# Kernel optimization log

Hardware: AMD Instinct MI355X
Metric: run time of the kernel (lower is better)

## Reference

```python
import jax, jax.numpy as jnp
import numpy as np

WINDOW_SIZE = 2
SOFTMAX_TEMP = 0.01


def get_indices(batch_size, window_size):
    # For each window, match keypoints of frame j against dense map of frame j+1.
    kp_inds, dense_inds = [], []
    for i in range(batch_size):
        for j in range(window_size - 1):
            idx = i * window_size + j
            kp_inds.append(idx)
            dense_inds.append(idx + 1)
    return np.array(kp_inds), np.array(dense_inds)


def l2_normalize(x, axis):
    n = jnp.sqrt(jnp.sum(x * x, axis=axis, keepdims=True))
    return x / jnp.maximum(n, 1e-12)


def grid_sample_bilinear(img, grid_u, grid_v):
    """torch.nn.functional.grid_sample, mode='bilinear', padding='zeros', align_corners=False.
    img: (B,C,H,W); grid_u, grid_v: (B,N) normalized coords in [-1,1]. Returns (B,C,N)."""
    B, C, H, W = img.shape
    x = ((grid_u + 1.0) * W - 1.0) * 0.5  # pixel x
    y = ((grid_v + 1.0) * H - 1.0) * 0.5  # pixel y
    x0 = jnp.floor(x)
    y0 = jnp.floor(y)
    wx1 = x - x0
    wy1 = y - y0
    flat = img.reshape(B, C, H * W)

    def gather(xi, yi):
        valid = (xi >= 0) & (xi <= W - 1) & (yi >= 0) & (yi <= H - 1)
        xi_c = jnp.clip(xi, 0, W - 1).astype(jnp.int32)
        yi_c = jnp.clip(yi, 0, H - 1).astype(jnp.int32)
        idx = yi_c * W + xi_c  # (B,N)
        vals = jnp.take_along_axis(flat, idx[:, None, :], axis=2)  # (B,C,N)
        return vals * valid[:, None, :].astype(img.dtype)

    out = (gather(x0, y0) * ((1 - wx1) * (1 - wy1))[:, None, :]
           + gather(x0 + 1, y0) * (wx1 * (1 - wy1))[:, None, :]
           + gather(x0, y0 + 1) * ((1 - wx1) * wy1)[:, None, :]
           + gather(x0 + 1, y0 + 1) * (wx1 * wy1)[:, None, :])
    return out


def setup_inputs() -> dict:
    key = jax.random.key(0)
    k1, k2, k3, k4 = jax.random.split(key, 4)
    BW, C, N, H, W = 8, 128, 512, 256, 256
    return {
        "keypoint_scores": jax.random.uniform(k1, (BW, 1, N), dtype=jnp.float32),
        "keypoint_desc": jax.random.normal(k2, (BW, C, N), dtype=jnp.float32),
        "scores_dense": jax.random.uniform(k3, (BW, 1, H, W), dtype=jnp.float32),
        "desc_dense": jax.random.normal(k4, (BW, C, H, W), dtype=jnp.float32),
    }


def reference(keypoint_scores, keypoint_desc, scores_dense, desc_dense):
    BW, C, N = keypoint_desc.shape
    batch_size = BW // WINDOW_SIZE
    _, _, H, W = desc_dense.shape
    kp_inds, dense_inds = get_indices(batch_size, WINDOW_SIZE)

    src_desc = l2_normalize(keypoint_desc[kp_inds], axis=1)  # (B,C,N)
    B = src_desc.shape[0]
    tgt_desc_dense = desc_dense[dense_inds]  # (B,C,H,W)
    tgt_unrolled = l2_normalize(tgt_desc_dense.reshape(B, C, H * W), axis=1)

    # cosine similarity scores (B,N,H*W) -> temperature softmax over dense map
    match_vals = jnp.einsum('bcn,bcm->bnm', src_desc, tgt_unrolled)
    soft_match_vals = jax.nn.softmax(match_vals / SOFTMAX_TEMP, axis=2)

    # soft-argmax: expected (u,v) pixel coordinates
    v_coord, u_coord = jnp.meshgrid(jnp.arange(H), jnp.arange(W), indexing='ij')
    coords = jnp.stack([u_coord.reshape(-1), v_coord.reshape(-1)], axis=1).astype(jnp.float32)  # (HW,2)
    pseudo_coords = jnp.einsum('bnm,mk->bnk', soft_match_vals, coords)  # (B,N,2)

    u_norm = 2.0 * pseudo_coords[:, :, 0] / (W - 1) - 1.0
    v_norm = 2.0 * pseudo_coords[:, :, 1] / (H - 1) - 1.0

    tgt_scores_dense = scores_dense[dense_inds]
    pseudo_scores = grid_sample_bilinear(tgt_scores_dense, u_norm, v_norm)  # (B,1,N)
    pseudo_desc = grid_sample_bilinear(tgt_desc_dense, u_norm, v_norm)      # (B,C,N)

    desc_match_score = jnp.sum(src_desc * pseudo_desc, axis=1, keepdims=True) / float(C)
    src_scores = keypoint_scores[kp_inds]
    match_weights = 0.5 * (desc_match_score + 1.0) * src_scores * pseudo_scores
    return (pseudo_coords, match_weights, soft_match_vals)
```

## Files before the change

kernel.cpp:

```cpp
#include <hip/hip_runtime.h>


typedef short  v8s __attribute__((ext_vector_type(8)));
typedef unsigned short v8u __attribute__((ext_vector_type(8)));
typedef float  v4f __attribute__((ext_vector_type(4)));

#define EXP2_SCALE 144.269504088896f
#define WAITV(N) asm volatile("s_waitcnt vmcnt(" #N ")" ::: "memory")
#define SBAR()   __builtin_amdgcn_s_barrier()
#define SCHED()  __builtin_amdgcn_sched_barrier(0)

static const size_t O_AHI  = 0;
static const size_t O_ALO  = O_AHI  + 262144ull*2;
static const size_t O_SRCN = O_ALO  + 262144ull*2;
static const size_t O_BHI  = O_SRCN + 262144ull*4;
static const size_t O_BLO  = O_BHI  + 33554432ull*2;
static const size_t O_PART = O_BLO  + 33554432ull*2;
static const size_t O_ROWS = O_PART + 2048ull*512*16;

static __device__ inline unsigned short f2bf(float x) {
    unsigned u = __float_as_uint(x);
    u = u + 0x7FFFu + ((u >> 16) & 1u);
    return (unsigned short)(u >> 16);
}
static __device__ inline float bf2f(unsigned short h) {
    return __uint_as_float(((unsigned)h) << 16);
}

__device__ __forceinline__ void gl_lds16(const void* g, void* l) {
    auto gp = (const __attribute__((address_space(1))) unsigned int*)(uintptr_t)g;
    auto lp = (__attribute__((address_space(3))) unsigned int*)(uintptr_t)l;
    __builtin_amdgcn_global_load_lds(gp, lp, 16, 0, 0);
}

__global__ void __launch_bounds__(256) k_prep_src(const float* __restrict__ kd,
                                                  float* __restrict__ srcN,
                                                  unsigned short* __restrict__ Ahi,
                                                  unsigned short* __restrict__ Alo) {
    int gw = blockIdx.x * 4 + (threadIdx.x >> 6);
    int l  = threadIdx.x & 63;
    int b  = gw >> 9, n = gw & 511;
    const float* base = kd + (size_t)(2 * b) * 128 * 512;
    float x0 = base[l * 512 + n];
    float x1 = base[(l + 64) * 512 + n];
    float ss = x0 * x0 + x1 * x1;
#pragma unroll
    for (int m = 1; m < 64; m <<= 1) ss += __shfl_xor(ss, m, 64);
    float inv = 1.0f / fmaxf(sqrtf(ss), 1e-12f);
    float xn0 = x0 * inv, xn1 = x1 * inv;
    int ob = gw * 128;
    srcN[ob + l] = xn0;  srcN[ob + l + 64] = xn1;
    unsigned short h0 = f2bf(xn0), h1 = f2bf(xn1);
    Ahi[ob + l] = h0;        Ahi[ob + l + 64] = h1;
    Alo[ob + l] = f2bf(xn0 - bf2f(h0));
    Alo[ob + l + 64] = f2bf(xn1 - bf2f(h1));
}

__global__ void __launch_bounds__(256) k_prep_tgt(const float* __restrict__ dd,
                                                  unsigned short* __restrict__ Bhi,
                                                  unsigned short* __restrict__ Blo) {
    int t = blockIdx.x * 128 + (threadIdx.x >> 1);
    int h = threadIdx.x & 1;
    int b = t >> 16;
    int p = t & 65535;
    const float* src = dd + (size_t)(2 * b + 1) * 128 * 65536 + (size_t)(h * 64) * 65536 + p;
    float v[64];
    float ss = 0.f;
#pragma unroll
    for (int c = 0; c < 64; ++c) { float x = src[(size_t)c * 65536]; v[c] = x; ss += x * x; }
    ss += __shfl_xor(ss, 1, 64);
    float inv = 1.0f / fmaxf(sqrtf(ss), 1e-12f);
    size_t ob = (size_t)t * 128 + h * 64;
#pragma unroll
    for (int c8 = 0; c8 < 8; ++c8) {
        v8u h8, l8;
#pragma unroll
        for (int j = 0; j < 8; ++j) {
            float xn = v[c8 * 8 + j] * inv;
            unsigned short hh = f2bf(xn);
            h8[j] = hh;
            l8[j] = f2bf(xn - bf2f(hh));
        }
        *(v8u*)(Bhi + ob + c8 * 8) = h8;
        *(v8u*)(Blo + ob + c8 * 8) = l8;
    }
}

template <int MODE>
__global__ void __launch_bounds__(512, 2) k_gemm(const unsigned short* __restrict__ Ahi,
                                                 const unsigned short* __restrict__ Alo,
                                                 const unsigned short* __restrict__ Bhi,
                                                 const unsigned short* __restrict__ Blo,
                                                 const float4* __restrict__ rows,
                                                 float* __restrict__ part,
                                                 float* __restrict__ out,
                                                 const float* __restrict__ ksc,
                                                 const float* __restrict__ sd,
                                                 const float* __restrict__ dd,
                                                 const float* __restrict__ srcN) {
    __shared__ v4f bstage4[6144];
    char* bstage = (char*)bstage4;

    const int tid = threadIdx.x;
    const int l = tid & 63, w = tid >> 6;
    const int wm = w >> 2, wn = w & 3;
    const int l15 = l & 15, l16 = l >> 4;
    const int mtg = blockIdx.x, ny = blockIdx.y, b = blockIdx.z;
    const int mt0 = mtg * 16;
    float* osm = out + 6144;

    v8s ahi[2][4], alo[2][4];
    {
        const size_t ar = ((size_t)(b * 512 + ny * 128 + wn * 32 + l15)) * 128 + l16 * 8;
#pragma unroll
        for (int nf = 0; nf < 2; ++nf)
#pragma unroll
            for (int ksl = 0; ksl < 4; ++ksl) {
                ahi[nf][ksl] = *(const v8s*)(Ahi + ar + nf * 2048 + ksl * 32);
                alo[nf][ksl] = *(const v8s*)(Alo + ar + nf * 2048 + ksl * 32);
            }
    }
    float invs[2];
    if (MODE == 1) {
#pragma unroll
        for (int nf = 0; nf < 2; ++nf)
            invs[nf] = rows[b * 512 + ny * 128 + wn * 32 + nf * 16 + l15].x;
    }
    WAITV(0);

    const size_t pxbase = ((size_t)b * 65536 + (size_t)mt0 * 128) * 128;

#define STAGEU(SRC, prow, bufidx)                                                   \
    {                                                                               \
        const unsigned short* src_ = (SRC) + (prow);                                \
        char* dst_ = bstage + (bufidx) * 32768;                                     \
        _Pragma("unroll")                                                           \
        for (int i = 0; i < 4; ++i) {                                               \
            int sl = tid + i * 512;                                                 \
            int rl = sl >> 4, gg = sl & 15;                                         \
            gl_lds16(src_ + rl * 128 + ((gg ^ (rl & 15)) << 3), dst_ + (sl << 4));  \
        }                                                                           \
    }
#define PXF(bufbase, mf_, ksl_)                                                     \
    (*(const v8s*)((bufbase) + (wm * 64 + (mf_) * 16 + l15) * 256 +                 \
                   ((((ksl_) * 4 + l16) ^ ((wm * 64 + (mf_) * 16 + l15) & 15)) << 4)))

    v4f acc[4][2];

    if (MODE == 0) {
        STAGEU(Bhi, pxbase, 0);
        STAGEU(Bhi, pxbase + 16384, 1);
#pragma unroll 1
        for (int mt = 0; mt < 16; ++mt) {
            if (mt < 14) STAGEU(Bhi, pxbase + (size_t)(mt + 2) * 16384, (mt + 2) % 3);
            if (mt == 0) WAITV(8);
            else if (mt == 1) WAITV(10);
            else if (mt == 14) WAITV(8);
            else if (mt == 15) WAITV(4);
            else WAITV(12);
            SBAR(); SCHED();
            const char* bb = bstage + (mt % 3) * 32768;
#pragma unroll
            for (int mf = 0; mf < 4; ++mf)
#pragma unroll
                for (int nf = 0; nf < 2; ++nf) { v4f z = {0.f,0.f,0.f,0.f}; acc[mf][nf] = z; }
#pragma unroll
            for (int ksl = 0; ksl < 4; ++ksl) {
                v8s pxf[4];
#pragma unroll
                for (int mf = 0; mf < 4; ++mf) pxf[mf] = PXF(bb, mf, ksl);
#pragma unroll
                for (int mf = 0; mf < 4; ++mf)
#pragma unroll
                    for (int nf = 0; nf < 2; ++nf) {
                        acc[mf][nf] = __builtin_amdgcn_mfma_f32_16x16x32_bf16(pxf[mf], ahi[nf][ksl], acc[mf][nf], 0, 0, 0);
                        acc[mf][nf] = __builtin_amdgcn_mfma_f32_16x16x32_bf16(pxf[mf], alo[nf][ksl], acc[mf][nf], 0, 0, 0);
                    }
            }
            SCHED();
            float sS[2] = {0.f, 0.f}, sM[2] = {0.f, 0.f};
#pragma unroll
            for (int mf = 0; mf < 4; ++mf) {
                int mloc = wm * 64 + mf * 16 + l16 * 4;
#pragma unroll
                for (int nf = 0; nf < 2; ++nf)
#pragma unroll
                    for (int r = 0; r < 4; ++r) {
                        float e = __builtin_amdgcn_exp2f(fmaf(acc[mf][nf][r], EXP2_SCALE, -EXP2_SCALE));
                        sS[nf] += e;
                        sM[nf] = fmaf(e, (float)(mloc + r), sM[nf]);
                    }
            }
#pragma unroll
            for (int nf = 0; nf < 2; ++nf) {
                sS[nf] += __shfl_xor(sS[nf], 16, 64); sS[nf] += __shfl_xor(sS[nf], 32, 64);
                sM[nf] += __shfl_xor(sM[nf], 16, 64); sM[nf] += __shfl_xor(sM[nf], 32, 64);
            }
            if (l < 16) {
#pragma unroll
                for (int nf = 0; nf < 2; ++nf) {
                    int row = b * 512 + ny * 128 + wn * 32 + nf * 16 + l15;
                    *(float2*)(part + (((size_t)row * 512 + (mt0 + mt)) * 2 + wm) * 2)
                        = make_float2(sS[nf], sM[nf]);
                }
            }
            SBAR();
        }
    } else {
        STAGEU(Bhi, pxbase, 0);
        STAGEU(Blo, pxbase, 1);
#pragma unroll 1
        for (int ph = 0; ph < 32; ++ph) {
            if (ph < 30) {
                size_t prow2 = pxbase + (size_t)((ph + 2) >> 1) * 16384;
                if ((ph & 1) == 0) STAGEU(Bhi, prow2, (ph + 2) % 3)
                else               STAGEU(Blo, prow2, (ph + 2) % 3)
            }
            if (ph <= 1) WAITV(8);
            else if (ph == 30) WAITV(12);
            else if (ph == 31) WAITV(8);
            else WAITV(16);
            SBAR(); SCHED();
            const char* bb = bstage + (ph % 3) * 32768;
            if ((ph & 1) == 0) {
#pragma unroll
                for (int mf = 0; mf < 4; ++mf)
#pragma unroll
                    for (int nf = 0; nf < 2; ++nf) { v4f z = {0.f,0.f,0.f,0.f}; acc[mf][nf] = z; }
#pragma unroll
                for (int ksl = 0; ksl < 4; ++ksl) {
                    v8s pxf[4];
#pragma unroll
                    for (int mf = 0; mf < 4; ++mf) pxf[mf] = PXF(bb, mf, ksl);
#pragma unroll
                    for (int mf = 0; mf < 4; ++mf)
#pragma unroll
                        for (int nf = 0; nf < 2; ++nf) {
                            acc[mf][nf] = __builtin_amdgcn_mfma_f32_16x16x32_bf16(pxf[mf], ahi[nf][ksl], acc[mf][nf], 0, 0, 0);
                            acc[mf][nf] = __builtin_amdgcn_mfma_f32_16x16x32_bf16(pxf[mf], alo[nf][ksl], acc[mf][nf], 0, 0, 0);
                        }
                }
                SCHED(); SBAR();
            } else {
#pragma unroll
                for (int ksl = 0; ksl < 4; ++ksl) {
                    v8s pxf[4];
#pragma unroll
                    for (int mf = 0; mf < 4; ++mf) pxf[mf] = PXF(bb, mf, ksl);
#pragma unroll
                    for (int mf = 0; mf < 4; ++mf)
#pragma unroll
                        for (int nf = 0; nf < 2; ++nf)
                            acc[mf][nf] = __builtin_amdgcn_mfma_f32_16x16x32_bf16(pxf[mf], ahi[nf][ksl], acc[mf][nf], 0, 0, 0);
                }
                SCHED();
                int mt = ph >> 1;
                size_t mg0 = (size_t)(mt0 + mt) * 128 + wm * 64 + l16 * 4;
#pragma unroll
                for (int mf = 0; mf < 4; ++mf)
#pragma unroll
                    for (int nf = 0; nf < 2; ++nf) {
                        v4f pv;
#pragma unroll
                        for (int r = 0; r < 4; ++r)
                            pv[r] = __builtin_amdgcn_exp2f(fmaf(acc[mf][nf][r], EXP2_SCALE, -EXP2_SCALE)) * invs[nf];
                        size_t ng = (size_t)(b * 512 + ny * 128 + wn * 32 + nf * 16 + l15);
                        __builtin_nontemporal_store(pv, (v4f*)(osm + ng * 65536 + mg0 + mf * 16));
                    }
                SBAR();
            }
        }

        if (w < 4) {
            const int bidx = mtg + 32 * ny + 128 * b;
            const int r = bidx * 4 + w;
            const int rb = r >> 9;
            float4 rs = rows[r];
            float u = rs.y, v = rs.z;
            float un = 2.0f * u / 255.0f - 1.0f;
            float vn = 2.0f * v / 255.0f - 1.0f;
            float x = ((un + 1.0f) * 256.0f - 1.0f) * 0.5f;
            float y = ((vn + 1.0f) * 256.0f - 1.0f) * 0.5f;
            float x0f = floorf(x), y0f = floorf(y);
            int x0 = (int)x0f, y0 = (int)y0f;
            int x1 = x0 + 1, y1 = y0 + 1;
            float wx1 = x - x0f, wy1 = y - y0f;
            float wx0 = 1.0f - wx1, wy0 = 1.0f - wy1;
            float m00 = ((x0 >= 0) & (x0 <= 255) & (y0 >= 0) & (y0 <= 255)) ? 1.f : 0.f;
            float m10 = ((x1 >= 0) & (x1 <= 255) & (y0 >= 0) & (y0 <= 255)) ? 1.f : 0.f;
            float m01 = ((x0 >= 0) & (x0 <= 255) & (y1 >= 0) & (y1 <= 255)) ? 1.f : 0.f;
            float m11 = ((x1 >= 0) & (x1 <= 255) & (y1 >= 0) & (y1 <= 255)) ? 1.f : 0.f;
            int cx0 = min(max(x0, 0), 255), cx1 = min(max(x1, 0), 255);
            int cy0 = min(max(y0, 0), 255), cy1 = min(max(y1, 0), 255);
            int i00 = cy0 * 256 + cx0, i10 = cy0 * 256 + cx1;
            int i01 = cy1 * 256 + cx0, i11 = cy1 * 256 + cx1;
            float w00 = wx0 * wy0 * m00, w10 = wx1 * wy0 * m10;
            float w01 = wx0 * wy1 * m01, w11 = wx1 * wy1 * m11;

            const float* sdb = sd + (size_t)(2 * rb + 1) * 65536;
            float ps = w00 * sdb[i00] + w10 * sdb[i10] + w01 * sdb[i01] + w11 * sdb[i11];

            const float* ddb = dd + (size_t)(2 * rb + 1) * 128 * 65536;
            float dot = 0.f;
#pragma unroll
            for (int h2 = 0; h2 < 2; ++h2) {
                int c = l + h2 * 64;
                const float* dc = ddb + (size_t)c * 65536;
                float pd = w00 * dc[i00] + w10 * dc[i10] + w01 * dc[i01] + w11 * dc[i11];
                dot += srcN[r * 128 + c] * pd;
            }
#pragma unroll
            for (int m = 1; m < 64; m <<= 1) dot += __shfl_xor(dot, m, 64);
            if (l == 0) {
                float dms = dot / 128.0f;
                float sscore = ksc[(2 * rb) * 512 + (r & 511)];
                out[4096 + r] = 0.5f * (dms + 1.0f) * sscore * ps;
            }
        }
    }
#undef STAGEU
#undef PXF
}

__global__ void __launch_bounds__(256) k_reduce(const float4* __restrict__ part,
                                                float4* __restrict__ rows,
                                                float* __restrict__ out) {
    int r = blockIdx.x * 4 + (threadIdx.x >> 6);
    int l = threadIdx.x & 63;
    float S = 0.f, Su = 0.f, Sv = 0.f;
#pragma unroll
    for (int i = 0; i < 8; ++i) {
        int mt = l + i * 64;
        float4 pp = part[(size_t)r * 512 + mt];
        float Sp = pp.x + pp.z;
        float Mp = pp.y + pp.w;
        S += Sp;
        Su += (float)((mt & 1) * 128) * Sp + Mp;
        Sv += (float)(mt >> 1) * Sp;
    }
#pragma unroll
    for (int m = 1; m < 64; m <<= 1) {
        S += __shfl_xor(S, m, 64);
        Su += __shfl_xor(Su, m, 64);
        Sv += __shfl_xor(Sv, m, 64);
    }
    if (l == 0) {
        float invS = 1.0f / S;
        float u = Su * invS, v = Sv * invS;
        rows[r] = make_float4(invS, u, v, 0.f);
        out[r * 2] = u;
        out[r * 2 + 1] = v;
    }
}

extern "C" void kernel_launch(void* const* d_in, const int* in_sizes, int n_in,
                              void* d_out, int out_size, void* d_ws, size_t ws_size,
                              hipStream_t stream) {
    const float* ksc = (const float*)d_in[0];
    const float* kd  = (const float*)d_in[1];
    const float* sd  = (const float*)d_in[2];
    const float* dd  = (const float*)d_in[3];
    float* out = (float*)d_out;
    char* ws = (char*)d_ws;

    unsigned short* Ahi  = (unsigned short*)(ws + O_AHI);
    unsigned short* Alo  = (unsigned short*)(ws + O_ALO);
    float*          srcN = (float*)(ws + O_SRCN);
    unsigned short* Bhi  = (unsigned short*)(ws + O_BHI);
    unsigned short* Blo  = (unsigned short*)(ws + O_BLO);
    float*          part = (float*)(ws + O_PART);
    float4*         rows = (float4*)(ws + O_ROWS);

    k_prep_src<<<512, 256, 0, stream>>>(kd, srcN, Ahi, Alo);
    k_prep_tgt<<<2048, 256, 0, stream>>>(dd, Bhi, Blo);
    k_gemm<0><<<dim3(32, 4, 4), 512, 0, stream>>>(Ahi, Alo, Bhi, Blo, rows, part, out, ksc, sd, dd, srcN);
    k_reduce<<<512, 256, 0, stream>>>((const float4*)part, rows, out);
    k_gemm<1><<<dim3(32, 4, 4), 512, 0, stream>>>(Ahi, Alo, Bhi, Blo, rows, part, out, ksc, sd, dd, srcN);
}
```

Baseline: 407.8 us.

## Use four-buffer LDS ring, in-register partial softmax sums, and MFMA priority

Both GEMM modes move from a three-buffer to a four-buffer LDS staging ring. The next tile is now issued after the barrier, which removes the trailing per-iteration barrier and loosens the vmcnt waits. In mode 0, softmax partial sums S/U/V now accumulate in registers across all 16 tiles and are written once per block, shrinking the partial buffer and the reduce kernel's reads. The mode 1 loop body is unified, and s_setprio is raised around the MFMA sections. The cost is more LDS per block, which could limit occupancy at two blocks per CU, and the loop now depends on fragile hand-tuned wait counts.

```diff
diff --git a/kernel.cpp b/kernel.cpp
--- a/kernel.cpp
+++ b/kernel.cpp
@@ -9,6 +9,7 @@
 #define WAITV(N) asm volatile("s_waitcnt vmcnt(" #N ")" ::: "memory")
 #define SBAR()   __builtin_amdgcn_s_barrier()
 #define SCHED()  __builtin_amdgcn_sched_barrier(0)
+#define PRIO(N)  __builtin_amdgcn_s_setprio(N)
 
 static const size_t O_AHI  = 0;
 static const size_t O_ALO  = O_AHI  + 262144ull*2;
@@ -16,7 +17,7 @@
 static const size_t O_BHI  = O_SRCN + 262144ull*4;
 static const size_t O_BLO  = O_BHI  + 33554432ull*2;
 static const size_t O_PART = O_BLO  + 33554432ull*2;
-static const size_t O_ROWS = O_PART + 2048ull*512*16;
+static const size_t O_ROWS = O_PART + 2048ull*64*16;
 
 static __device__ inline unsigned short f2bf(float x) {
     unsigned u = __float_as_uint(x);
@@ -98,7 +99,7 @@
                                                  const float* __restrict__ sd,
                                                  const float* __restrict__ dd,
                                                  const float* __restrict__ srcN) {
-    __shared__ v4f bstage4[6144];
+    __shared__ v4f bstage4[8192];
     char* bstage = (char*)bstage4;
 
     const int tid = threadIdx.x;
@@ -130,9 +131,9 @@
 
     const size_t pxbase = ((size_t)b * 65536 + (size_t)mt0 * 128) * 128;
 
-#define STAGEU(SRC, prow, bufidx)                                                   \
+#define STAGEU(SRC, eoff, bufidx)                                                   \
     {                                                                               \
-        const unsigned short* src_ = (SRC) + (prow);                                \
+        const unsigned short* src_ = (SRC) + pxbase + (eoff);                       \
         char* dst_ = bstage + (bufidx) * 32768;                                     \
         _Pragma("unroll")                                                           \
         for (int i = 0; i < 4; ++i) {                                               \
@@ -148,22 +149,20 @@
     v4f acc[4][2];
 
     if (MODE == 0) {
-        STAGEU(Bhi, pxbase, 0);
-        STAGEU(Bhi, pxbase + 16384, 1);
+        float sS[2] = {0.f, 0.f}, sU[2] = {0.f, 0.f}, sV[2] = {0.f, 0.f};
+        STAGEU(Bhi, 0, 0);
+        STAGEU(Bhi, 16384, 1);
 #pragma unroll 1
         for (int mt = 0; mt < 16; ++mt) {
-            if (mt < 14) STAGEU(Bhi, pxbase + (size_t)(mt + 2) * 16384, (mt + 2) % 3);
-            if (mt == 0) WAITV(8);
-            else if (mt == 1) WAITV(10);
-            else if (mt == 14) WAITV(8);
-            else if (mt == 15) WAITV(4);
-            else WAITV(12);
+            if (mt == 15) WAITV(0); else WAITV(4);
             SBAR(); SCHED();
-            const char* bb = bstage + (mt % 3) * 32768;
+            if (mt < 14) STAGEU(Bhi, (size_t)(mt + 2) * 16384, (mt + 2) & 3);
+            const char* bb = bstage + (mt & 3) * 32768;
 #pragma unroll
             for (int mf = 0; mf < 4; ++mf)
 #pragma unroll
                 for (int nf = 0; nf < 2; ++nf) { v4f z = {0.f,0.f,0.f,0.f}; acc[mf][nf] = z; }
+            PRIO(1);
 #pragma unroll
             for (int ksl = 0; ksl < 4; ++ksl) {
                 v8s pxf[4];
@@ -177,8 +176,10 @@
                         acc[mf][nf] = __builtin_amdgcn_mfma_f32_16x16x32_bf16(pxf[mf], alo[nf][ksl], acc[mf][nf], 0, 0, 0);
                     }
             }
+            PRIO(0);
             SCHED();
-            float sS[2] = {0.f, 0.f}, sM[2] = {0.f, 0.f};
+            const int mtv = mt0 + mt;
+            float ts[2] = {0.f, 0.f};
 #pragma unroll
             for (int mf = 0; mf < 4; ++mf) {
                 int mloc = wm * 64 + mf * 16 + l16 * 4;
@@ -187,73 +188,72 @@
 #pragma unroll
                     for (int r = 0; r < 4; ++r) {
                         float e = __builtin_amdgcn_exp2f(fmaf(acc[mf][nf][r], EXP2_SCALE, -EXP2_SCALE));
-                        sS[nf] += e;
-                        sM[nf] = fmaf(e, (float)(mloc + r), sM[nf]);
+                        ts[nf] += e;
+                        sU[nf] = fmaf(e, (float)(mloc + r), sU[nf]);
                     }
             }
 #pragma unroll
             for (int nf = 0; nf < 2; ++nf) {
-                sS[nf] += __shfl_xor(sS[nf], 16, 64); sS[nf] += __shfl_xor(sS[nf], 32, 64);
-                sM[nf] += __shfl_xor(sM[nf], 16, 64); sM[nf] += __shfl_xor(sM[nf], 32, 64);
-            }
-            if (l < 16) {
-#pragma unroll
-                for (int nf = 0; nf < 2; ++nf) {
-                    int row = b * 512 + ny * 128 + wn * 32 + nf * 16 + l15;
-                    *(float2*)(part + (((size_t)row * 512 + (mt0 + mt)) * 2 + wm) * 2)
-                        = make_float2(sS[nf], sM[nf]);
-                }
-            }
-            SBAR();
+                sS[nf] += ts[nf];
+                sV[nf] = fmaf(ts[nf], (float)(mtv >> 1), sV[nf]);
+                if (mtv & 1) sU[nf] = fmaf(ts[nf], 128.f, sU[nf]);
+            }
+        }
+#pragma unroll
+        for (int nf = 0; nf < 2; ++nf) {
+            sS[nf] += __shfl_xor(sS[nf], 16, 64); sS[nf] += __shfl_xor(sS[nf], 32, 64);
+            sU[nf] += __shfl_xor(sU[nf], 16, 64); sU[nf] += __shfl_xor(sU[nf], 32, 64);
+            sV[nf] += __shfl_xor(sV[nf], 16, 64); sV[nf] += __shfl_xor(sV[nf], 32, 64);
+        }
+        if (l < 16) {
+#pragma unroll
+            for (int nf = 0; nf < 2; ++nf) {
+                int row = b * 512 + ny * 128 + wn * 32 + nf * 16 + l15;
+                ((float4*)part)[((size_t)row * 32 + mtg) * 2 + wm]
+                    = make_float4(sS[nf], sU[nf], sV[nf], 0.f);
+            }
         }
     } else {
-        STAGEU(Bhi, pxbase, 0);
-        STAGEU(Blo, pxbase, 1);
+        STAGEU(Bhi, 0, 0);
+        STAGEU(Blo, 0, 1);
 #pragma unroll 1
         for (int ph = 0; ph < 32; ++ph) {
+            if (ph <= 1) WAITV(4);
+            else if (ph == 31) WAITV(8);
+            else WAITV(12);
+            SBAR(); SCHED();
             if (ph < 30) {
-                size_t prow2 = pxbase + (size_t)((ph + 2) >> 1) * 16384;
-                if ((ph & 1) == 0) STAGEU(Bhi, prow2, (ph + 2) % 3)
-                else               STAGEU(Blo, prow2, (ph + 2) % 3)
-            }
-            if (ph <= 1) WAITV(8);
-            else if (ph == 30) WAITV(12);
-            else if (ph == 31) WAITV(8);
-            else WAITV(16);
-            SBAR(); SCHED();
-            const char* bb = bstage + (ph % 3) * 32768;
-            if ((ph & 1) == 0) {
+                const int pn = ph + 2;
+                const size_t eoff = (size_t)(pn >> 1) * 16384;
+                if ((pn & 1) == 0) STAGEU(Bhi, eoff, pn & 3)
+                else               STAGEU(Blo, eoff, pn & 3)
+            }
+            const char* bb = bstage + (ph & 3) * 32768;
+            const int sub = ph & 1;
+            if (sub == 0) {
 #pragma unroll
                 for (int mf = 0; mf < 4; ++mf)
 #pragma unroll
                     for (int nf = 0; nf < 2; ++nf) { v4f z = {0.f,0.f,0.f,0.f}; acc[mf][nf] = z; }
-#pragma unroll
-                for (int ksl = 0; ksl < 4; ++ksl) {
-                    v8s pxf[4];
-#pragma unroll
-                    for (int mf = 0; mf < 4; ++mf) pxf[mf] = PXF(bb, mf, ksl);
-#pragma unroll
-                    for (int mf = 0; mf < 4; ++mf)
-#pragma unroll
-                        for (int nf = 0; nf < 2; ++nf) {
-                            acc[mf][nf] = __builtin_amdgcn_mfma_f32_16x16x32_bf16(pxf[mf], ahi[nf][ksl], acc[mf][nf], 0, 0, 0);
+            }
+            PRIO(1);
+#pragma unroll
+            for (int ksl = 0; ksl < 4; ++ksl) {
+                v8s pxf[4];
+#pragma unroll
+                for (int mf = 0; mf < 4; ++mf) pxf[mf] = PXF(bb, mf, ksl);
+#pragma unroll
+                for (int mf = 0; mf < 4; ++mf)
+#pragma unroll
+                    for (int nf = 0; nf < 2; ++nf) {
+                        acc[mf][nf] = __builtin_amdgcn_mfma_f32_16x16x32_bf16(pxf[mf], ahi[nf][ksl], acc[mf][nf], 0, 0, 0);
+                        if (sub == 0)
                             acc[mf][nf] = __builtin_amdgcn_mfma_f32_16x16x32_bf16(pxf[mf], alo[nf][ksl], acc[mf][nf], 0, 0, 0);
-                        }
-                }
-                SCHED(); SBAR();
-            } else {
-#pragma unroll
-                for (int ksl = 0; ksl < 4; ++ksl) {
-                    v8s pxf[4];
-#pragma unroll
-                    for (int mf = 0; mf < 4; ++mf) pxf[mf] = PXF(bb, mf, ksl);
-#pragma unroll
-                    for (int mf = 0; mf < 4; ++mf)
-#pragma unroll
-                        for (int nf = 0; nf < 2; ++nf)
-                            acc[mf][nf] = __builtin_amdgcn_mfma_f32_16x16x32_bf16(pxf[mf], ahi[nf][ksl], acc[mf][nf], 0, 0, 0);
-                }
-                SCHED();
+                    }
+            }
+            PRIO(0);
+            SCHED();
+            if (sub == 1) {
                 int mt = ph >> 1;
                 size_t mg0 = (size_t)(mt0 + mt) * 128 + wm * 64 + l16 * 4;
 #pragma unroll
@@ -267,7 +267,6 @@
                         size_t ng = (size_t)(b * 512 + ny * 128 + wn * 32 + nf * 16 + l15);
                         __builtin_nontemporal_store(pv, (v4f*)(osm + ng * 65536 + mg0 + mf * 16));
                     }
-                SBAR();
             }
         }
 
@@ -327,17 +326,8 @@
                                                 float* __restrict__ out) {
     int r = blockIdx.x * 4 + (threadIdx.x >> 6);
     int l = threadIdx.x & 63;
-    float S = 0.f, Su = 0.f, Sv = 0.f;
-#pragma unroll
-    for (int i = 0; i < 8; ++i) {
-        int mt = l + i * 64;
-        float4 pp = part[(size_t)r * 512 + mt];
-        float Sp = pp.x + pp.z;
-        float Mp = pp.y + pp.w;
-        S += Sp;
-        Su += (float)((mt & 1) * 128) * Sp + Mp;
-        Sv += (float)(mt >> 1) * Sp;
-    }
+    float4 pp = part[(size_t)r * 64 + l];
+    float S = pp.x, Su = pp.y, Sv = pp.z;
 #pragma unroll
     for (int m = 1; m < 64; m <<= 1) {
         S += __shfl_xor(S, m, 64);
```

After: 387.1 us. 1.05x faster.
